# Kernel optimization log

Measured on AMD Instinct MI355X. Metric: run time of the kernel, lower is better.

The kernel has to match this reference:

```python
import jax, jax.numpy as jnp
import numpy as np

N, E, D = 100000, 640000, 128  # nodes, edges, feature dim (in_dim == out_dim == 128)
BN_EPS = 1e-5


def setup_inputs() -> dict:
    key = jax.random.key(0)
    ks = jax.random.split(key, 8)
    x = jax.random.normal(ks[0], (N, D), dtype=jnp.float32)
    edge_index = jax.random.randint(ks[1], (2, E), 0, N, dtype=jnp.int64)
    s = 1.0 / np.sqrt(D)
    W1 = jax.random.uniform(ks[2], (D, D), jnp.float32, -s, s)
    b1 = jax.random.uniform(ks[3], (D,), jnp.float32, -s, s)
    W2 = jax.random.uniform(ks[4], (D, D), jnp.float32, -s, s)
    b2 = jax.random.uniform(ks[5], (D,), jnp.float32, -s, s)
    return {
        "x": x,
        "edge_index": edge_index,
        "eps": jnp.array([0.1], dtype=jnp.float32),
        "W1": W1, "b1": b1,
        "g1": jnp.ones((D,), jnp.float32), "beta1": jnp.zeros((D,), jnp.float32),
        "W2": W2, "b2": b2,
        "g2": jnp.ones((D,), jnp.float32), "beta2": jnp.zeros((D,), jnp.float32),
    }


def _batchnorm(h, gamma, beta):
    # BatchNorm1d in training mode: biased batch stats over the node dim
    mean = jnp.mean(h, axis=0)
    var = jnp.var(h, axis=0)
    return gamma * (h - mean) * jax.lax.rsqrt(var + BN_EPS) + beta


def reference(x, edge_index, eps, W1, b1, g1, beta1, W2, b2, g2, beta2):
    src, dst = edge_index[0], edge_index[1]
    # gather messages from source nodes, scatter-add into destination nodes
    aggr = jax.ops.segment_sum(x[src], dst, num_segments=x.shape[0])  # [N, D]
    h = (1.0 + eps) * x + aggr
    h = jax.nn.relu(_batchnorm(h @ W1.T + b1, g1, beta1))
    h = jax.nn.relu(_batchnorm(h @ W2.T + b2, g2, beta2))
    return h
```

## Files before the change

### kernel.cpp

```cpp
#include <hip/hip_runtime.h>

#define NN 100000
#define DD 128
#define EE 640000
#define NPAD 100352

typedef __bf16 bf16x8 __attribute__((ext_vector_type(8)));
typedef float floatx4 __attribute__((ext_vector_type(4)));

union BF8 {
    bf16x8 v;
    unsigned short u[8];
    int4 i4;
};

__device__ __forceinline__ unsigned short f2bf(float f) {
    unsigned int u = __float_as_uint(f);
    u += 0x7FFF + ((u >> 16) & 1);
    return (unsigned short)(u >> 16);
}

__global__ __launch_bounds__(256) void hist_k(const int* __restrict__ ei,
                                              int* __restrict__ deg) {
    int e = blockIdx.x * 256 + threadIdx.x;
    if (e < EE) atomicAdd(&deg[ei[EE + e]], 1);
}

__global__ __launch_bounds__(256) void scan1_k(const int* __restrict__ deg,
                                               int* __restrict__ exc,
                                               int* __restrict__ chunkSums) {
    __shared__ int s[256];
    int t = threadIdx.x, g = blockIdx.x * 256 + t;
    int v = (g < NN) ? deg[g] : 0;
    s[t] = v;
    __syncthreads();
    for (int off = 1; off < 256; off <<= 1) {
        int u = (t >= off) ? s[t - off] : 0;
        __syncthreads();
        s[t] += u;
        __syncthreads();
    }
    if (g < NN) exc[g] = s[t] - v;
    if (t == 255) chunkSums[blockIdx.x] = s[255];
}

__global__ __launch_bounds__(512) void scan2_k(int* __restrict__ chunkSums, int n) {
    __shared__ int s[512];
    int t = threadIdx.x;
    int v = (t < n) ? chunkSums[t] : 0;
    s[t] = v;
    __syncthreads();
    for (int off = 1; off < 512; off <<= 1) {
        int u = (t >= off) ? s[t - off] : 0;
        __syncthreads();
        s[t] += u;
        __syncthreads();
    }
    if (t < n) chunkSums[t] = s[t] - v;
}

__global__ __launch_bounds__(256) void scan3_k(int* __restrict__ exc,
                                               const int* __restrict__ chunkSums,
                                               int* __restrict__ cursor) {
    int g = blockIdx.x * 256 + threadIdx.x;
    if (g < NN) {
        int o = exc[g] + chunkSums[blockIdx.x];
        exc[g] = o;
        cursor[g] = o;
    }
}

__global__ __launch_bounds__(256) void esort_k(const int* __restrict__ ei,
                                               int* __restrict__ cursor,
                                               int* __restrict__ ssrc) {
    int e = blockIdx.x * 256 + threadIdx.x;
    if (e >= EE) return;
    int pos = atomicAdd(&cursor[ei[EE + e]], 1);
    ssrc[pos] = ei[e];
}

__global__ __launch_bounds__(256) void wconv_k(const float* __restrict__ W1,
                                               const float* __restrict__ W2,
                                               unsigned short* __restrict__ wb) {
    int i = blockIdx.x * 256 + threadIdx.x;
    const float4* s4 = (i < 4096) ? (const float4*)W1 : (const float4*)W2;
    float4 v = s4[i & 4095];
    ushort4 u;
    u.x = f2bf(v.x); u.y = f2bf(v.y); u.z = f2bf(v.z); u.w = f2bf(v.w);
    ((ushort4*)wb)[i] = u;
}

__global__ __launch_bounds__(256, 4) void aggregate_k(
    const float4* __restrict__ x4, const int* __restrict__ ssrc,
    const int* __restrict__ offs, const int* __restrict__ deg,
    const float* __restrict__ epsp, ushort4* __restrict__ hout) {
    int tid = blockIdx.x * 256 + threadIdx.x;
    int node = tid >> 5, lane = tid & 31;
    if (node >= NN) return;
    int start = offs[node], d = deg[node];
    float ef = 1.0f + epsp[0];
    float4 v = x4[node * 32 + lane];
    float ax = ef * v.x, ay = ef * v.y, az = ef * v.z, aw = ef * v.w;
    for (int j = 0; j < d; j += 8) {
        int r = d - j;
        int b = start + j;
        int s0 = ssrc[b];
        int s1 = ssrc[b + ((r > 1) ? 1 : 0)];
        int s2 = ssrc[b + ((r > 2) ? 2 : 0)];
        int s3 = ssrc[b + ((r > 3) ? 3 : 0)];
        int s4i = ssrc[b + ((r > 4) ? 4 : 0)];
        int s5 = ssrc[b + ((r > 5) ? 5 : 0)];
        int s6 = ssrc[b + ((r > 6) ? 6 : 0)];
        int s7 = ssrc[b + ((r > 7) ? 7 : 0)];
        float4 x0 = x4[s0 * 32 + lane];
        float4 x1 = x4[s1 * 32 + lane];
        float4 x2 = x4[s2 * 32 + lane];
        float4 x3 = x4[s3 * 32 + lane];
        float4 x4v = x4[s4i * 32 + lane];
        float4 x5 = x4[s5 * 32 + lane];
        float4 x6 = x4[s6 * 32 + lane];
        float4 x7 = x4[s7 * 32 + lane];
        float m1 = (r > 1) ? 1.f : 0.f;
        float m2 = (r > 2) ? 1.f : 0.f;
        float m3 = (r > 3) ? 1.f : 0.f;
        float m4 = (r > 4) ? 1.f : 0.f;
        float m5 = (r > 5) ? 1.f : 0.f;
        float m6 = (r > 6) ? 1.f : 0.f;
        float m7 = (r > 7) ? 1.f : 0.f;
        ax += x0.x; ay += x0.y; az += x0.z; aw += x0.w;
        ax += m1 * x1.x; ay += m1 * x1.y; az += m1 * x1.z; aw += m1 * x1.w;
        ax += m2 * x2.x; ay += m2 * x2.y; az += m2 * x2.z; aw += m2 * x2.w;
        ax += m3 * x3.x; ay += m3 * x3.y; az += m3 * x3.z; aw += m3 * x3.w;
        ax += m4 * x4v.x; ay += m4 * x4v.y; az += m4 * x4v.z; aw += m4 * x4v.w;
        ax += m5 * x5.x; ay += m5 * x5.y; az += m5 * x5.z; aw += m5 * x5.w;
        ax += m6 * x6.x; ay += m6 * x6.y; az += m6 * x6.z; aw += m6 * x6.w;
        ax += m7 * x7.x; ay += m7 * x7.y; az += m7 * x7.z; aw += m7 * x7.w;
    }
    ushort4 u;
    u.x = f2bf(ax); u.y = f2bf(ay); u.z = f2bf(az); u.w = f2bf(aw);
    hout[node * 32 + lane] = u;
}

template <int FUSE_BN>
__global__ __launch_bounds__(256, 2) void gin_gemm_k(
    const unsigned short* __restrict__ hin,
    const float* __restrict__ yin,
    const float* __restrict__ statsIn,
    const float* __restrict__ gmm,
    const float* __restrict__ bta,
    const unsigned short* __restrict__ Wbf, const float* __restrict__ bias,
    float* __restrict__ y, float* __restrict__ statsOut) {
    __shared__ __align__(16) float s_sum[128];
    __shared__ __align__(16) float s_sq[128];
    __shared__ __align__(16) float sc[128];
    __shared__ __align__(16) float sh[128];
    __shared__ __align__(16) float yst[4][16][132];

    const int tid = threadIdx.x;
    const int l = tid & 63, w = tid >> 6;
    const int m = l & 15, q = l >> 4;

    if (tid < 128) {
        s_sum[tid] = 0.f;
        s_sq[tid] = 0.f;
        if (FUSE_BN) {
            const float inv = 1.0f / (float)NN;
            float mean = statsIn[tid] * inv;
            float var = statsIn[128 + tid] * inv - mean * mean;
            float s = gmm[tid] * rsqrtf(var + 1e-5f);
            sc[tid] = s;
            sh[tid] = bta[tid] - mean * s;
        }
    }

    bf16x8 wf[8][4];
#pragma unroll
    for (int ct = 0; ct < 8; ++ct) {
        const unsigned short* wr = Wbf + (size_t)(ct * 16 + m) * 128 + q * 8;
#pragma unroll
        for (int kc = 0; kc < 4; ++kc) {
            BF8 t;
            t.i4 = *(const int4*)(wr + kc * 32);
            wf[ct][kc] = t.v;
        }
    }
    float bc[8];
#pragma unroll
    for (int ct = 0; ct < 8; ++ct) bc[ct] = bias[ct * 16 + m];

    float ps[8], pq[8];
#pragma unroll
    for (int ct = 0; ct < 8; ++ct) { ps[ct] = 0.f; pq[ct] = 0.f; }

    __syncthreads();

    const int NT = NN / 16;
    const int stride = gridDim.x * 4;
    int t = blockIdx.x * 4 + w;

    const unsigned short* abase = hin + (size_t)m * 128 + q * 8;
    const float* ybase = yin + (size_t)m * 128 + q * 8;

    int4 ra[4];
    float4 rf[8];
    if (t < NT) {
        if (FUSE_BN) {
            const float* yp = ybase + (size_t)t * (16 * 128);
#pragma unroll
            for (int i = 0; i < 8; ++i)
                rf[i] = *(const float4*)(yp + (i >> 1) * 32 + (i & 1) * 4);
        } else {
            const unsigned short* ap = abase + (size_t)t * (16 * 128);
#pragma unroll
            for (int kc = 0; kc < 4; ++kc) ra[kc] = *(const int4*)(ap + kc * 32);
        }
    }

    while (t < NT) {
        bf16x8 a[4];
#pragma unroll
        for (int kc = 0; kc < 4; ++kc) {
            if (FUSE_BN) {
                float4 v0 = rf[2 * kc], v1 = rf[2 * kc + 1];
                float4 s0 = *(const float4*)(sc + kc * 32 + q * 8);
                float4 s1 = *(const float4*)(sc + kc * 32 + q * 8 + 4);
                float4 h0 = *(const float4*)(sh + kc * 32 + q * 8);
                float4 h1 = *(const float4*)(sh + kc * 32 + q * 8 + 4);
                BF8 tt;
                tt.u[0] = f2bf(fmaxf(v0.x * s0.x + h0.x, 0.f));
                tt.u[1] = f2bf(fmaxf(v0.y * s0.y + h0.y, 0.f));
                tt.u[2] = f2bf(fmaxf(v0.z * s0.z + h0.z, 0.f));
                tt.u[3] = f2bf(fmaxf(v0.w * s0.w + h0.w, 0.f));
                tt.u[4] = f2bf(fmaxf(v1.x * s1.x + h1.x, 0.f));
                tt.u[5] = f2bf(fmaxf(v1.y * s1.y + h1.y, 0.f));
                tt.u[6] = f2bf(fmaxf(v1.z * s1.z + h1.z, 0.f));
                tt.u[7] = f2bf(fmaxf(v1.w * s1.w + h1.w, 0.f));
                a[kc] = tt.v;
            } else {
                BF8 tt;
                tt.i4 = ra[kc];
                a[kc] = tt.v;
            }
        }

        int tn = t + stride;
        if (tn < NT) {
            if (FUSE_BN) {
                const float* yp = ybase + (size_t)tn * (16 * 128);
#pragma unroll
                for (int i = 0; i < 8; ++i)
                    rf[i] = *(const float4*)(yp + (i >> 1) * 32 + (i & 1) * 4);
            } else {
                const unsigned short* ap = abase + (size_t)tn * (16 * 128);
#pragma unroll
                for (int kc = 0; kc < 4; ++kc) ra[kc] = *(const int4*)(ap + kc * 32);
            }
        }

        floatx4 acc[8];
#pragma unroll
        for (int ct = 0; ct < 8; ++ct) acc[ct] = (floatx4)0.0f;
#pragma unroll
        for (int kc = 0; kc < 4; ++kc)
#pragma unroll
            for (int ct = 0; ct < 8; ++ct)
                acc[ct] = __builtin_amdgcn_mfma_f32_16x16x32_bf16(a[kc], wf[ct][kc], acc[ct], 0, 0, 0);

#pragma unroll
        for (int ct = 0; ct < 8; ++ct) {
#pragma unroll
            for (int i = 0; i < 4; ++i) {
                float yv = acc[ct][i] + bc[ct];
                yst[w][q * 4 + i][ct * 16 + m] = yv;
                ps[ct] += yv;
                pq[ct] += yv * yv;
            }
        }
        asm volatile("s_waitcnt lgkmcnt(0)" ::: "memory");
        float* yb = y + (size_t)t * (16 * 128);
#pragma unroll
        for (int it = 0; it < 8; ++it) {
            int f4 = it * 64 + l;
            int row = f4 >> 5, c4 = f4 & 31;
            float4 vv = *(const float4*)&yst[w][row][c4 * 4];
            *(float4*)(yb + row * 128 + c4 * 4) = vv;
        }
        t = tn;
    }

#pragma unroll
    for (int ct = 0; ct < 8; ++ct) {
        atomicAdd(&s_sum[ct * 16 + m], ps[ct]);
        atomicAdd(&s_sq[ct * 16 + m], pq[ct]);
    }
    __syncthreads();
    if (tid < 128) {
        unsafeAtomicAdd(&statsOut[tid], s_sum[tid]);
        unsafeAtomicAdd(&statsOut[128 + tid], s_sq[tid]);
    }
}

__global__ __launch_bounds__(256) void bn_relu_k(
    const float* __restrict__ y, const float* __restrict__ stats,
    const float* __restrict__ g, const float* __restrict__ beta,
    float* __restrict__ outf) {
    __shared__ __align__(16) float sc[128];
    __shared__ __align__(16) float sh[128];
    int t = threadIdx.x;
    if (t < 128) {
        const float inv = 1.0f / (float)NN;
        float mean = stats[t] * inv;
        float var = stats[128 + t] * inv - mean * mean;
        float s = g[t] * rsqrtf(var + 1e-5f);
        sc[t] = s;
        sh[t] = beta[t] - mean * s;
    }
    __syncthreads();
    const int total4 = NN * 32;
    const float4* y4 = (const float4*)y;
    for (int i = blockIdx.x * 256 + t; i < total4; i += gridDim.x * 256) {
        int c4 = i & 31;
        float4 v = y4[i];
        float4 s = ((const float4*)sc)[c4];
        float4 b = ((const float4*)sh)[c4];
        float r0 = fmaxf(v.x * s.x + b.x, 0.f);
        float r1 = fmaxf(v.y * s.y + b.y, 0.f);
        float r2 = fmaxf(v.z * s.z + b.z, 0.f);
        float r3 = fmaxf(v.w * s.w + b.w, 0.f);
        ((float4*)outf)[i] = make_float4(r0, r1, r2, r3);
    }
}

extern "C" void kernel_launch(void* const* d_in, const int* in_sizes, int n_in,
                              void* d_out, int out_size, void* d_ws, size_t ws_size,
                              hipStream_t stream) {
    const float* x   = (const float*)d_in[0];
    const int* ei    = (const int*)d_in[1];
    const float* eps = (const float*)d_in[2];
    const float* W1  = (const float*)d_in[3];
    const float* b1  = (const float*)d_in[4];
    const float* g1  = (const float*)d_in[5];
    const float* be1 = (const float*)d_in[6];
    const float* W2  = (const float*)d_in[7];
    const float* b2  = (const float*)d_in[8];
    const float* g2  = (const float*)d_in[9];
    const float* be2 = (const float*)d_in[10];
    float* out = (float*)d_out;

    int* deg        = (int*)d_ws;
    int* offs       = deg + NPAD;
    int* cursor     = offs + NPAD;
    int* chunkSums  = cursor + NPAD;
    int* ssrc       = chunkSums + 512;
    unsigned short* hbuf = (unsigned short*)(ssrc + EE + 256);
    float* stats    = (float*)(hbuf + (size_t)NN * DD);
    unsigned short* wbf = (unsigned short*)(stats + 512);

    hipMemsetAsync(deg, 0, NPAD * sizeof(int), stream);
    hipMemsetAsync(stats, 0, 512 * sizeof(float), stream);

    const int numChunks = (NN + 255) / 256;
    hist_k<<<(EE + 255) / 256, 256, 0, stream>>>(ei, deg);
    scan1_k<<<numChunks, 256, 0, stream>>>(deg, offs, chunkSums);
    scan2_k<<<1, 512, 0, stream>>>(chunkSums, numChunks);
    scan3_k<<<numChunks, 256, 0, stream>>>(offs, chunkSums, cursor);
    esort_k<<<(EE + 255) / 256, 256, 0, stream>>>(ei, cursor, ssrc);
    aggregate_k<<<(NN * 32 + 255) / 256, 256, 0, stream>>>(
        (const float4*)x, ssrc, offs, deg, eps, (ushort4*)hbuf);
    wconv_k<<<32, 256, 0, stream>>>(W1, W2, wbf);

    const int gblocks = 512;
    gin_gemm_k<0><<<gblocks, 256, 0, stream>>>(
        hbuf, nullptr, nullptr, nullptr, nullptr, wbf, b1, out, stats);
    gin_gemm_k<1><<<gblocks, 256, 0, stream>>>(
        nullptr, out, stats, g1, be1, wbf + 16384, b2, out, stats + 256);
    bn_relu_k<<<4096, 256, 0, stream>>>(out, stats + 256, g2, be2, out);
}
```

Measured before the change: 322.8 us.

## Fuse CSR build, aggregation and MLP stages into two cooperative persistent kernels

The separate histogram, scan, edge sort, weight conversion and aggregation kernels, plus both memsets, are merged into one cooperative kernel that uses grid-wide syncs between phases. The two GEMM+BN stages and the final BN+ReLU become a second cooperative kernel with grid syncs between them. This removes roughly ten kernel launches and their inter-kernel gaps. In exchange it adds grid-barrier costs and a grid size fixed by the occupancy query, which may leave scatter/gather phases less parallel than the old per-element launches.

```diff
diff --git a/kernel.cpp b/kernel.cpp
--- a/kernel.cpp
+++ b/kernel.cpp
@@ -1,9 +1,13 @@
 #include <hip/hip_runtime.h>
+#include <hip/hip_cooperative_groups.h>
+
+namespace cg = cooperative_groups;
 
 #define NN 100000
 #define DD 128
 #define EE 640000
 #define NPAD 100352
+#define NCHUNK 391
 
 typedef __bf16 bf16x8 __attribute__((ext_vector_type(8)));
 typedef float floatx4 __attribute__((ext_vector_type(4)));
@@ -20,142 +24,140 @@
     return (unsigned short)(u >> 16);
 }
 
-__global__ __launch_bounds__(256) void hist_k(const int* __restrict__ ei,
-                                              int* __restrict__ deg) {
-    int e = blockIdx.x * 256 + threadIdx.x;
-    if (e < EE) atomicAdd(&deg[ei[EE + e]], 1);
-}
-
-__global__ __launch_bounds__(256) void scan1_k(const int* __restrict__ deg,
-                                               int* __restrict__ exc,
-                                               int* __restrict__ chunkSums) {
-    __shared__ int s[256];
-    int t = threadIdx.x, g = blockIdx.x * 256 + t;
-    int v = (g < NN) ? deg[g] : 0;
-    s[t] = v;
-    __syncthreads();
-    for (int off = 1; off < 256; off <<= 1) {
-        int u = (t >= off) ? s[t - off] : 0;
+__global__ __launch_bounds__(256, 8) void build_agg_k(
+    const int* __restrict__ ei, const float4* __restrict__ x4,
+    const float* __restrict__ epsp,
+    const float* __restrict__ W1, const float* __restrict__ W2,
+    int* __restrict__ deg, int* __restrict__ offs, int* __restrict__ cursor,
+    int* __restrict__ chunkSums, int* __restrict__ ssrc,
+    ushort4* __restrict__ hout, unsigned short* __restrict__ wbf,
+    float* __restrict__ stats) {
+    cg::grid_group gg = cg::this_grid();
+    const int tid = threadIdx.x;
+    const int g0 = blockIdx.x * 256 + tid;
+    const int gsz = gridDim.x * 256;
+    __shared__ int s[512];
+
+    for (int i = g0; i < NPAD; i += gsz) deg[i] = 0;
+    if (g0 < 512) stats[g0] = 0.f;
+    gg.sync();
+
+    for (int e = g0; e < EE; e += gsz) atomicAdd(&deg[ei[EE + e]], 1);
+    gg.sync();
+
+    for (int c = blockIdx.x; c < NCHUNK; c += gridDim.x) {
+        int g = c * 256 + tid;
+        int v = (g < NN) ? deg[g] : 0;
+        s[tid] = v;
         __syncthreads();
-        s[t] += u;
+        for (int off = 1; off < 256; off <<= 1) {
+            int u = (tid >= off) ? s[tid - off] : 0;
+            __syncthreads();
+            s[tid] += u;
+            __syncthreads();
+        }
+        if (g < NN) offs[g] = s[tid] - v;
+        if (tid == 255) chunkSums[c] = s[255];
         __syncthreads();
     }
-    if (g < NN) exc[g] = s[t] - v;
-    if (t == 255) chunkSums[blockIdx.x] = s[255];
-}
-
-__global__ __launch_bounds__(512) void scan2_k(int* __restrict__ chunkSums, int n) {
-    __shared__ int s[512];
-    int t = threadIdx.x;
-    int v = (t < n) ? chunkSums[t] : 0;
-    s[t] = v;
-    __syncthreads();
-    for (int off = 1; off < 512; off <<= 1) {
-        int u = (t >= off) ? s[t - off] : 0;
+    gg.sync();
+
+    if (blockIdx.x == 0) {
+        int v0 = (2 * tid < NCHUNK) ? chunkSums[2 * tid] : 0;
+        int v1 = (2 * tid + 1 < NCHUNK) ? chunkSums[2 * tid + 1] : 0;
+        int pair = v0 + v1;
+        s[tid] = pair;
         __syncthreads();
-        s[t] += u;
-        __syncthreads();
-    }
-    if (t < n) chunkSums[t] = s[t] - v;
-}
-
-__global__ __launch_bounds__(256) void scan3_k(int* __restrict__ exc,
-                                               const int* __restrict__ chunkSums,
-                                               int* __restrict__ cursor) {
-    int g = blockIdx.x * 256 + threadIdx.x;
-    if (g < NN) {
-        int o = exc[g] + chunkSums[blockIdx.x];
-        exc[g] = o;
+        for (int off = 1; off < 256; off <<= 1) {
+            int u = (tid >= off) ? s[tid - off] : 0;
+            __syncthreads();
+            s[tid] += u;
+            __syncthreads();
+        }
+        int excPair = s[tid] - pair;
+        if (2 * tid < NCHUNK) chunkSums[2 * tid] = excPair;
+        if (2 * tid + 1 < NCHUNK) chunkSums[2 * tid + 1] = excPair + v0;
+    }
+    gg.sync();
+
+    for (int g = g0; g < NN; g += gsz) {
+        int o = offs[g] + chunkSums[g >> 8];
+        offs[g] = o;
         cursor[g] = o;
     }
-}
-
-__global__ __launch_bounds__(256) void esort_k(const int* __restrict__ ei,
-                                               int* __restrict__ cursor,
-                                               int* __restrict__ ssrc) {
-    int e = blockIdx.x * 256 + threadIdx.x;
-    if (e >= EE) return;
-    int pos = atomicAdd(&cursor[ei[EE + e]], 1);
-    ssrc[pos] = ei[e];
-}
-
-__global__ __launch_bounds__(256) void wconv_k(const float* __restrict__ W1,
-                                               const float* __restrict__ W2,
-                                               unsigned short* __restrict__ wb) {
-    int i = blockIdx.x * 256 + threadIdx.x;
-    const float4* s4 = (i < 4096) ? (const float4*)W1 : (const float4*)W2;
-    float4 v = s4[i & 4095];
-    ushort4 u;
-    u.x = f2bf(v.x); u.y = f2bf(v.y); u.z = f2bf(v.z); u.w = f2bf(v.w);
-    ((ushort4*)wb)[i] = u;
-}
-
-__global__ __launch_bounds__(256, 4) void aggregate_k(
-    const float4* __restrict__ x4, const int* __restrict__ ssrc,
-    const int* __restrict__ offs, const int* __restrict__ deg,
-    const float* __restrict__ epsp, ushort4* __restrict__ hout) {
-    int tid = blockIdx.x * 256 + threadIdx.x;
-    int node = tid >> 5, lane = tid & 31;
-    if (node >= NN) return;
-    int start = offs[node], d = deg[node];
-    float ef = 1.0f + epsp[0];
-    float4 v = x4[node * 32 + lane];
-    float ax = ef * v.x, ay = ef * v.y, az = ef * v.z, aw = ef * v.w;
-    for (int j = 0; j < d; j += 8) {
-        int r = d - j;
-        int b = start + j;
-        int s0 = ssrc[b];
-        int s1 = ssrc[b + ((r > 1) ? 1 : 0)];
-        int s2 = ssrc[b + ((r > 2) ? 2 : 0)];
-        int s3 = ssrc[b + ((r > 3) ? 3 : 0)];
-        int s4i = ssrc[b + ((r > 4) ? 4 : 0)];
-        int s5 = ssrc[b + ((r > 5) ? 5 : 0)];
-        int s6 = ssrc[b + ((r > 6) ? 6 : 0)];
-        int s7 = ssrc[b + ((r > 7) ? 7 : 0)];
-        float4 x0 = x4[s0 * 32 + lane];
-        float4 x1 = x4[s1 * 32 + lane];
-        float4 x2 = x4[s2 * 32 + lane];
-        float4 x3 = x4[s3 * 32 + lane];
-        float4 x4v = x4[s4i * 32 + lane];
-        float4 x5 = x4[s5 * 32 + lane];
-        float4 x6 = x4[s6 * 32 + lane];
-        float4 x7 = x4[s7 * 32 + lane];
-        float m1 = (r > 1) ? 1.f : 0.f;
-        float m2 = (r > 2) ? 1.f : 0.f;
-        float m3 = (r > 3) ? 1.f : 0.f;
-        float m4 = (r > 4) ? 1.f : 0.f;
-        float m5 = (r > 5) ? 1.f : 0.f;
-        float m6 = (r > 6) ? 1.f : 0.f;
-        float m7 = (r > 7) ? 1.f : 0.f;
-        ax += x0.x; ay += x0.y; az += x0.z; aw += x0.w;
-        ax += m1 * x1.x; ay += m1 * x1.y; az += m1 * x1.z; aw += m1 * x1.w;
-        ax += m2 * x2.x; ay += m2 * x2.y; az += m2 * x2.z; aw += m2 * x2.w;
-        ax += m3 * x3.x; ay += m3 * x3.y; az += m3 * x3.z; aw += m3 * x3.w;
-        ax += m4 * x4v.x; ay += m4 * x4v.y; az += m4 * x4v.z; aw += m4 * x4v.w;
-        ax += m5 * x5.x; ay += m5 * x5.y; az += m5 * x5.z; aw += m5 * x5.w;
-        ax += m6 * x6.x; ay += m6 * x6.y; az += m6 * x6.z; aw += m6 * x6.w;
-        ax += m7 * x7.x; ay += m7 * x7.y; az += m7 * x7.z; aw += m7 * x7.w;
-    }
-    ushort4 u;
-    u.x = f2bf(ax); u.y = f2bf(ay); u.z = f2bf(az); u.w = f2bf(aw);
-    hout[node * 32 + lane] = u;
+    gg.sync();
+
+    for (int e = g0; e < EE; e += gsz) {
+        int pos = atomicAdd(&cursor[ei[EE + e]], 1);
+        ssrc[pos] = ei[e];
+    }
+    gg.sync();
+
+    for (int i = g0; i < 8192; i += gsz) {
+        const float4* s4 = (i < 4096) ? (const float4*)W1 : (const float4*)W2;
+        float4 v = s4[i & 4095];
+        ushort4 u;
+        u.x = f2bf(v.x); u.y = f2bf(v.y); u.z = f2bf(v.z); u.w = f2bf(v.w);
+        ((ushort4*)wbf)[i] = u;
+    }
+
+    const int lane = tid & 31;
+    const int grpStride = gsz >> 5;
+    const float ef = 1.0f + epsp[0];
+    for (int node = g0 >> 5; node < NN; node += grpStride) {
+        int start = offs[node], d = deg[node];
+        float4 v = x4[node * 32 + lane];
+        float ax = ef * v.x, ay = ef * v.y, az = ef * v.z, aw = ef * v.w;
+        for (int j = 0; j < d; j += 8) {
+            int r = d - j;
+            int b = start + j;
+            int s0 = ssrc[b];
+            int s1 = ssrc[b + ((r > 1) ? 1 : 0)];
+            int s2 = ssrc[b + ((r > 2) ? 2 : 0)];
+            int s3 = ssrc[b + ((r > 3) ? 3 : 0)];
+            int s4i = ssrc[b + ((r > 4) ? 4 : 0)];
+            int s5 = ssrc[b + ((r > 5) ? 5 : 0)];
+            int s6 = ssrc[b + ((r > 6) ? 6 : 0)];
+            int s7 = ssrc[b + ((r > 7) ? 7 : 0)];
+            float4 x0 = x4[s0 * 32 + lane];
+            float4 x1 = x4[s1 * 32 + lane];
+            float4 x2 = x4[s2 * 32 + lane];
+            float4 x3 = x4[s3 * 32 + lane];
+            float4 x4v = x4[s4i * 32 + lane];
+            float4 x5 = x4[s5 * 32 + lane];
+            float4 x6 = x4[s6 * 32 + lane];
+            float4 x7 = x4[s7 * 32 + lane];
+            float m1 = (r > 1) ? 1.f : 0.f;
+            float m2 = (r > 2) ? 1.f : 0.f;
+            float m3 = (r > 3) ? 1.f : 0.f;
+            float m4 = (r > 4) ? 1.f : 0.f;
+            float m5 = (r > 5) ? 1.f : 0.f;
+            float m6 = (r > 6) ? 1.f : 0.f;
+            float m7 = (r > 7) ? 1.f : 0.f;
+            ax += x0.x; ay += x0.y; az += x0.z; aw += x0.w;
+            ax += m1 * x1.x; ay += m1 * x1.y; az += m1 * x1.z; aw += m1 * x1.w;
+            ax += m2 * x2.x; ay += m2 * x2.y; az += m2 * x2.z; aw += m2 * x2.w;
+            ax += m3 * x3.x; ay += m3 * x3.y; az += m3 * x3.z; aw += m3 * x3.w;
+            ax += m4 * x4v.x; ay += m4 * x4v.y; az += m4 * x4v.z; aw += m4 * x4v.w;
+            ax += m5 * x5.x; ay += m5 * x5.y; az += m5 * x5.z; aw += m5 * x5.w;
+            ax += m6 * x6.x; ay += m6 * x6.y; az += m6 * x6.z; aw += m6 * x6.w;
+            ax += m7 * x7.x; ay += m7 * x7.y; az += m7 * x7.z; aw += m7 * x7.w;
+        }
+        ushort4 u;
+        u.x = f2bf(ax); u.y = f2bf(ay); u.z = f2bf(az); u.w = f2bf(aw);
+        hout[node * 32 + lane] = u;
+    }
 }
 
 template <int FUSE_BN>
-__global__ __launch_bounds__(256, 2) void gin_gemm_k(
-    const unsigned short* __restrict__ hin,
-    const float* __restrict__ yin,
-    const float* __restrict__ statsIn,
-    const float* __restrict__ gmm,
-    const float* __restrict__ bta,
-    const unsigned short* __restrict__ Wbf, const float* __restrict__ bias,
-    float* __restrict__ y, float* __restrict__ statsOut) {
-    __shared__ __align__(16) float s_sum[128];
-    __shared__ __align__(16) float s_sq[128];
-    __shared__ __align__(16) float sc[128];
-    __shared__ __align__(16) float sh[128];
-    __shared__ __align__(16) float yst[4][16][132];
-
+__device__ __forceinline__ void gemm_body(
+    const unsigned short* __restrict__ hin, const float* __restrict__ yin,
+    const float* __restrict__ statsIn, const float* __restrict__ gmm,
+    const float* __restrict__ bta, const unsigned short* __restrict__ Wbf,
+    const float* __restrict__ bias, float* __restrict__ y,
+    float* __restrict__ statsOut, float* __restrict__ s_sum,
+    float* __restrict__ s_sq, float* __restrict__ sc, float* __restrict__ sh,
+    float* __restrict__ yst) {
     const int tid = threadIdx.x;
     const int l = tid & 63, w = tid >> 6;
     const int m = l & 15, q = l >> 4;
@@ -167,9 +169,9 @@
             const float inv = 1.0f / (float)NN;
             float mean = statsIn[tid] * inv;
             float var = statsIn[128 + tid] * inv - mean * mean;
-            float s = gmm[tid] * rsqrtf(var + 1e-5f);
-            sc[tid] = s;
-            sh[tid] = bta[tid] - mean * s;
+            float sv = gmm[tid] * rsqrtf(var + 1e-5f);
+            sc[tid] = sv;
+            sh[tid] = bta[tid] - mean * sv;
         }
     }
 
@@ -215,6 +217,8 @@
             for (int kc = 0; kc < 4; ++kc) ra[kc] = *(const int4*)(ap + kc * 32);
         }
     }
+
+    float* ytile = yst + w * (16 * 132);
 
     while (t < NT) {
         bf16x8 a[4];
@@ -271,7 +275,7 @@
 #pragma unroll
             for (int i = 0; i < 4; ++i) {
                 float yv = acc[ct][i] + bc[ct];
-                yst[w][q * 4 + i][ct * 16 + m] = yv;
+                ytile[(q * 4 + i) * 132 + ct * 16 + m] = yv;
                 ps[ct] += yv;
                 pq[ct] += yv * yv;
             }
@@ -282,7 +286,7 @@
         for (int it = 0; it < 8; ++it) {
             int f4 = it * 64 + l;
             int row = f4 >> 5, c4 = f4 & 31;
-            float4 vv = *(const float4*)&yst[w][row][c4 * 4];
+            float4 vv = *(const float4*)&ytile[row * 132 + c4 * 4];
             *(float4*)(yb + row * 128 + c4 * 4) = vv;
         }
         t = tn;
@@ -300,41 +304,54 @@
     }
 }
 
-__global__ __launch_bounds__(256) void bn_relu_k(
-    const float* __restrict__ y, const float* __restrict__ stats,
-    const float* __restrict__ g, const float* __restrict__ beta,
-    float* __restrict__ outf) {
+__global__ __launch_bounds__(256, 2) void mlp_k(
+    const unsigned short* __restrict__ hbuf,
+    const unsigned short* __restrict__ wbf,
+    const float* __restrict__ b1, const float* __restrict__ g1,
+    const float* __restrict__ be1, const float* __restrict__ b2,
+    const float* __restrict__ g2, const float* __restrict__ be2,
+    float* __restrict__ out, float* __restrict__ stats) {
+    cg::grid_group gg = cg::this_grid();
+    __shared__ __align__(16) float s_sum[128];
+    __shared__ __align__(16) float s_sq[128];
     __shared__ __align__(16) float sc[128];
     __shared__ __align__(16) float sh[128];
-    int t = threadIdx.x;
-    if (t < 128) {
+    __shared__ __align__(16) float yst[4 * 16 * 132];
+
+    gemm_body<0>(hbuf, nullptr, nullptr, nullptr, nullptr, wbf, b1, out, stats,
+                 s_sum, s_sq, sc, sh, yst);
+    gg.sync();
+    gemm_body<1>(nullptr, out, stats, g1, be1, wbf + 16384, b2, out,
+                 stats + 256, s_sum, s_sq, sc, sh, yst);
+    gg.sync();
+
+    const int tid = threadIdx.x;
+    if (tid < 128) {
         const float inv = 1.0f / (float)NN;
-        float mean = stats[t] * inv;
-        float var = stats[128 + t] * inv - mean * mean;
-        float s = g[t] * rsqrtf(var + 1e-5f);
-        sc[t] = s;
-        sh[t] = beta[t] - mean * s;
+        float mean = stats[256 + tid] * inv;
+        float var = stats[384 + tid] * inv - mean * mean;
+        float sv = g2[tid] * rsqrtf(var + 1e-5f);
+        sc[tid] = sv;
+        sh[tid] = be2[tid] - mean * sv;
     }
     __syncthreads();
     const int total4 = NN * 32;
-    const float4* y4 = (const float4*)y;
-    for (int i = blockIdx.x * 256 + t; i < total4; i += gridDim.x * 256) {
+    float4* y4 = (float4*)out;
+    for (int i = blockIdx.x * 256 + tid; i < total4; i += gridDim.x * 256) {
         int c4 = i & 31;
         float4 v = y4[i];
-        float4 s = ((const float4*)sc)[c4];
-        float4 b = ((const float4*)sh)[c4];
-        float r0 = fmaxf(v.x * s.x + b.x, 0.f);
-        float r1 = fmaxf(v.y * s.y + b.y, 0.f);
-        float r2 = fmaxf(v.z * s.z + b.z, 0.f);
-        float r3 = fmaxf(v.w * s.w + b.w, 0.f);
-        ((float4*)outf)[i] = make_float4(r0, r1, r2, r3);
+        float4 sv = ((const float4*)sc)[c4];
+        float4 bv = ((const float4*)sh)[c4];
+        y4[i] = make_float4(fmaxf(v.x * sv.x + bv.x, 0.f),
+                            fmaxf(v.y * sv.y + bv.y, 0.f),
+                            fmaxf(v.z * sv.z + bv.z, 0.f),
+                            fmaxf(v.w * sv.w + bv.w, 0.f));
     }
 }
 
 extern "C" void kernel_launch(void* const* d_in, const int* in_sizes, int n_in,
                               void* d_out, int out_size, void* d_ws, size_t ws_size,
                               hipStream_t stream) {
-    const float* x   = (const float*)d_in[0];
     const int* ei    = (const int*)d_in[1];
     const float* eps = (const float*)d_in[2];
     const float* W1  = (const float*)d_in[3];
@@ -345,6 +362,7 @@
     const float* b2  = (const float*)d_in[8];
     const float* g2  = (const float*)d_in[9];
     const float* be2 = (const float*)d_in[10];
+    const float4* x4 = (const float4*)d_in[0];
     float* out = (float*)d_out;
 
     int* deg        = (int*)d_ws;
@@ -355,24 +373,24 @@
     unsigned short* hbuf = (unsigned short*)(ssrc + EE + 256);
     float* stats    = (float*)(hbuf + (size_t)NN * DD);
     unsigned short* wbf = (unsigned short*)(stats + 512);
-
-    hipMemsetAsync(deg, 0, NPAD * sizeof(int), stream);
-    hipMemsetAsync(stats, 0, 512 * sizeof(float), stream);
-
-    const int numChunks = (NN + 255) / 256;
-    hist_k<<<(EE + 255) / 256, 256, 0, stream>>>(ei, deg);
-    scan1_k<<<numChunks, 256, 0, stream>>>(deg, offs, chunkSums);
-    scan2_k<<<1, 512, 0, stream>>>(chunkSums, numChunks);
-    scan3_k<<<numChunks, 256, 0, stream>>>(offs, chunkSums, cursor);
-    esort_k<<<(EE + 255) / 256, 256, 0, stream>>>(ei, cursor, ssrc);
-    aggregate_k<<<(NN * 32 + 255) / 256, 256, 0, stream>>>(
-        (const float4*)x, ssrc, offs, deg, eps, (ushort4*)hbuf);
-    wconv_k<<<32, 256, 0, stream>>>(W1, W2, wbf);
-
-    const int gblocks = 512;
-    gin_gemm_k<0><<<gblocks, 256, 0, stream>>>(
-        hbuf, nullptr, nullptr, nullptr, nullptr, wbf, b1, out, stats);
-    gin_gemm_k<1><<<gblocks, 256, 0, stream>>>(
-        nullptr, out, stats, g1, be1, wbf + 16384, b2, out, stats + 256);
-    bn_relu_k<<<4096, 256, 0, stream>>>(out, stats + 256, g2, be2, out);
-}
+    ushort4* hout   = (ushort4*)hbuf;
+
+    int nbA = 0, nbB = 0;
+    if (hipOccupancyMaxActiveBlocksPerMultiprocessor(&nbA, build_agg_k, 256, 0) != hipSuccess || nbA < 1) nbA = 4;
+    if (hipOccupancyMaxActiveBlocksPerMultiprocessor(&nbB, mlp_k, 256, 0) != hipSuccess || nbB < 1) nbB = 2;
+    if (nbA > 8) nbA = 8;
+    if (nbB > 8) nbB = 8;
+    dim3 blk(256);
+    dim3 gridA(nbA * 256);
+    dim3 gridB(nbB * 256);
+
+    void* argsA[] = {(void*)&ei, (void*)&x4, (void*)&eps, (void*)&W1, (void*)&W2,
+                     (void*)&deg, (void*)&offs, (void*)&cursor, (void*)&chunkSums,
+                     (void*)&ssrc, (void*)&hout, (void*)&wbf, (void*)&stats};
+    hipLaunchCooperativeKernel(build_agg_k, gridA, blk, argsA, 0, stream);
+
+    void* argsB[] = {(void*)&hbuf, (void*)&wbf, (void*)&b1, (void*)&g1,
+                     (void*)&be1, (void*)&b2, (void*)&g2, (void*)&be2,
+                     (void*)&out, (void*)&stats};
+    hipLaunchCooperativeKernel(mlp_k, gridB, blk, argsB, 0, stream);
+}
```

Result: slower. 965.9 us (+199.2%).

## Replace three-pass scan with decoupled look-back scan and fold weight conversion into esort

Applied to the files above, without the earlier changes.

Merges the three scan kernels into one single-pass decoupled look-back scan, where each chunk publishes its aggregate and inclusive prefix through flag-tagged descriptors. The weight bf16 conversion and the stats zeroing are moved into extra blocks of the edge-sort kernel, and the two memsets become one. This cuts the number of kernel launches and memsets on a short pipeline. The look-back spin relies on earlier blocks being scheduled first, which is a forward-progress assumption that holds for a grid this small.

```diff
diff --git a/kernel.cpp b/kernel.cpp
--- a/kernel.cpp
+++ b/kernel.cpp
@@ -4,6 +4,7 @@
 #define DD 128
 #define EE 640000
 #define NPAD 100352
+#define NCHUNK 391
 
 typedef __bf16 bf16x8 __attribute__((ext_vector_type(8)));
 typedef float floatx4 __attribute__((ext_vector_type(4)));
@@ -26,11 +27,13 @@
     if (e < EE) atomicAdd(&deg[ei[EE + e]], 1);
 }
 
-__global__ __launch_bounds__(256) void scan1_k(const int* __restrict__ deg,
-                                               int* __restrict__ exc,
-                                               int* __restrict__ chunkSums) {
+__global__ __launch_bounds__(256) void scanlb_k(
+    const int* __restrict__ deg, unsigned int* __restrict__ descr,
+    int* __restrict__ offs, int* __restrict__ cursor) {
     __shared__ int s[256];
-    int t = threadIdx.x, g = blockIdx.x * 256 + t;
+    __shared__ int sbase;
+    const int c = blockIdx.x, t = threadIdx.x;
+    int g = c * 256 + t;
     int v = (g < NN) ? deg[g] : 0;
     s[t] = v;
     __syncthreads();
@@ -40,54 +43,60 @@
         s[t] += u;
         __syncthreads();
     }
-    if (g < NN) exc[g] = s[t] - v;
-    if (t == 255) chunkSums[blockIdx.x] = s[255];
-}
-
-__global__ __launch_bounds__(512) void scan2_k(int* __restrict__ chunkSums, int n) {
-    __shared__ int s[512];
-    int t = threadIdx.x;
-    int v = (t < n) ? chunkSums[t] : 0;
-    s[t] = v;
-    __syncthreads();
-    for (int off = 1; off < 512; off <<= 1) {
-        int u = (t >= off) ? s[t - off] : 0;
-        __syncthreads();
-        s[t] += u;
-        __syncthreads();
-    }
-    if (t < n) chunkSums[t] = s[t] - v;
-}
-
-__global__ __launch_bounds__(256) void scan3_k(int* __restrict__ exc,
-                                               const int* __restrict__ chunkSums,
-                                               int* __restrict__ cursor) {
-    int g = blockIdx.x * 256 + threadIdx.x;
+    const int total = s[255];
+    if (t == 0) {
+        if (c == 0) {
+            __hip_atomic_store(&descr[0], (2u << 30) | (unsigned)total,
+                               __ATOMIC_RELEASE, __HIP_MEMORY_SCOPE_AGENT);
+            sbase = 0;
+        } else {
+            __hip_atomic_store(&descr[c], (1u << 30) | (unsigned)total,
+                               __ATOMIC_RELEASE, __HIP_MEMORY_SCOPE_AGENT);
+            int acc = 0, p = c - 1;
+            while (true) {
+                unsigned st = __hip_atomic_load(&descr[p], __ATOMIC_ACQUIRE,
+                                                __HIP_MEMORY_SCOPE_AGENT);
+                unsigned fl = st >> 30;
+                if (fl == 0u) continue;
+                acc += (int)(st & 0x3FFFFFFFu);
+                if (fl == 2u) break;
+                --p;
+            }
+            __hip_atomic_store(&descr[c], (2u << 30) | (unsigned)(acc + total),
+                               __ATOMIC_RELEASE, __HIP_MEMORY_SCOPE_AGENT);
+            sbase = acc;
+        }
+    }
+    __syncthreads();
     if (g < NN) {
-        int o = exc[g] + chunkSums[blockIdx.x];
-        exc[g] = o;
+        int o = sbase + s[t] - v;
+        offs[g] = o;
         cursor[g] = o;
     }
 }
 
-__global__ __launch_bounds__(256) void esort_k(const int* __restrict__ ei,
-                                               int* __restrict__ cursor,
-                                               int* __restrict__ ssrc) {
-    int e = blockIdx.x * 256 + threadIdx.x;
-    if (e >= EE) return;
+__global__ __launch_bounds__(256) void esort_k(
+    const int* __restrict__ ei, int* __restrict__ cursor,
+    int* __restrict__ ssrc, const float* __restrict__ W1,
+    const float* __restrict__ W2, unsigned short* __restrict__ wbf,
+    float* __restrict__ stats) {
+    int b = blockIdx.x;
+    if (b >= 2500) {
+        int i = (b - 2500) * 256 + threadIdx.x;
+        if (b == 2500) {
+            stats[threadIdx.x] = 0.f;
+            stats[256 + threadIdx.x] = 0.f;
+        }
+        const float4* s4 = (i < 4096) ? (const float4*)W1 : (const float4*)W2;
+        float4 v = s4[i & 4095];
+        ushort4 u;
+        u.x = f2bf(v.x); u.y = f2bf(v.y); u.z = f2bf(v.z); u.w = f2bf(v.w);
+        ((ushort4*)wbf)[i] = u;
+        return;
+    }
+    int e = b * 256 + threadIdx.x;
     int pos = atomicAdd(&cursor[ei[EE + e]], 1);
     ssrc[pos] = ei[e];
-}
-
-__global__ __launch_bounds__(256) void wconv_k(const float* __restrict__ W1,
-                                               const float* __restrict__ W2,
-                                               unsigned short* __restrict__ wb) {
-    int i = blockIdx.x * 256 + threadIdx.x;
-    const float4* s4 = (i < 4096) ? (const float4*)W1 : (const float4*)W2;
-    float4 v = s4[i & 4095];
-    ushort4 u;
-    u.x = f2bf(v.x); u.y = f2bf(v.y); u.z = f2bf(v.z); u.w = f2bf(v.w);
-    ((ushort4*)wb)[i] = u;
 }
 
 __global__ __launch_bounds__(256, 4) void aggregate_k(
@@ -347,27 +356,22 @@
     const float* be2 = (const float*)d_in[10];
     float* out = (float*)d_out;
 
-    int* deg        = (int*)d_ws;
-    int* offs       = deg + NPAD;
-    int* cursor     = offs + NPAD;
-    int* chunkSums  = cursor + NPAD;
-    int* ssrc       = chunkSums + 512;
+    int* deg            = (int*)d_ws;
+    unsigned int* descr = (unsigned int*)(deg + NPAD);
+    int* offs           = (int*)(descr + 512);
+    int* cursor         = offs + NPAD;
+    int* ssrc           = cursor + NPAD;
     unsigned short* hbuf = (unsigned short*)(ssrc + EE + 256);
-    float* stats    = (float*)(hbuf + (size_t)NN * DD);
+    float* stats        = (float*)(hbuf + (size_t)NN * DD);
     unsigned short* wbf = (unsigned short*)(stats + 512);
 
-    hipMemsetAsync(deg, 0, NPAD * sizeof(int), stream);
-    hipMemsetAsync(stats, 0, 512 * sizeof(float), stream);
-
-    const int numChunks = (NN + 255) / 256;
+    hipMemsetAsync(deg, 0, (NPAD + 512) * sizeof(int), stream);
+
     hist_k<<<(EE + 255) / 256, 256, 0, stream>>>(ei, deg);
-    scan1_k<<<numChunks, 256, 0, stream>>>(deg, offs, chunkSums);
-    scan2_k<<<1, 512, 0, stream>>>(chunkSums, numChunks);
-    scan3_k<<<numChunks, 256, 0, stream>>>(offs, chunkSums, cursor);
-    esort_k<<<(EE + 255) / 256, 256, 0, stream>>>(ei, cursor, ssrc);
+    scanlb_k<<<NCHUNK, 256, 0, stream>>>(deg, descr, offs, cursor);
+    esort_k<<<2500 + 32, 256, 0, stream>>>(ei, cursor, ssrc, W1, W2, wbf, stats);
     aggregate_k<<<(NN * 32 + 255) / 256, 256, 0, stream>>>(
         (const float4*)x, ssrc, offs, deg, eps, (ushort4*)hbuf);
-    wconv_k<<<32, 256, 0, stream>>>(W1, W2, wbf);
 
     const int gblocks = 512;
     gin_gemm_k<0><<<gblocks, 256, 0, stream>>>(
```

Result: slower. 409.7 us (+26.9%).
